# Kernel optimization log

Hardware: AMD Instinct MI355X
Metric: run time of the kernel (lower is better)

The kernel has to match this reference:

```python
import jax, jax.numpy as jnp
import numpy as np

N = 4096      # number of mesh points
H = 64        # hidden_dim
K = 15        # k_neighbors
E = 32768     # explicit input edges


def _knn_edges(points, k):
    # dense pairwise squared distances [N,N]; exclude self via +inf diagonal
    sq = jnp.sum(points * points, axis=1)
    d2 = sq[:, None] - 2.0 * (points @ points.T) + sq[None, :]
    n = points.shape[0]
    d2 = d2.at[jnp.arange(n), jnp.arange(n)].set(jnp.inf)
    _, idx = jax.lax.top_k(-d2, k)              # [N,k] nearest neighbor ids
    src = jnp.repeat(jnp.arange(n), k)          # node i
    dst = idx.reshape(-1)                       # its neighbors
    return src, dst


def setup_inputs() -> dict:
    key = jax.random.key(0)
    ks = jax.random.split(key, 8)
    points = jax.random.normal(ks[0], (N, 3), jnp.float32)
    features = jax.random.normal(ks[1], (N, H), jnp.float32)
    edge_index = jax.random.randint(ks[2], (2, E), 0, N)

    def lin(k, fin, fout):
        k1, k2 = jax.random.split(k)
        s = 1.0 / np.sqrt(fin)
        W = jax.random.uniform(k1, (fout, fin), jnp.float32, -s, s)
        b = jax.random.uniform(k2, (fout,), jnp.float32, -s, s)
        return W, b

    W_theta, b_theta = lin(ks[3], 3, H)
    W_phi, b_phi = lin(ks[4], H, H)
    W_q, b_q = lin(ks[5], H, H)
    W_k, b_k = lin(ks[6], H, H)
    return dict(points=points, features=features, edge_index=edge_index,
                W_theta=W_theta, b_theta=b_theta, W_phi=W_phi, b_phi=b_phi,
                W_q=W_q, b_q=b_q, W_k=W_k, b_k=b_k)


def reference(points, features, edge_index, W_theta, b_theta, W_phi, b_phi,
              W_q, b_q, W_k, b_k):
    n = points.shape[0]
    # extended edge list = explicit edges + KNN edges (src = node, dst = neighbor)
    src_knn, dst_knn = _knn_edges(points, K)
    src = jnp.concatenate([edge_index[0], src_knn])
    dst = jnp.concatenate([edge_index[1], dst_knn])

    # per-node max-pooled edge MLP: max_j W_theta(p_j - p_i), then ReLU(W_phi(.))
    diff = points[dst] - points[src]                     # [M,3]
    h = diff @ W_theta.T + b_theta                       # [M,H]
    max_feat = jax.ops.segment_max(h, src, num_segments=n)  # [N,H] (every node has >=K nbrs)
    dev = jax.nn.relu(max_feat @ W_phi.T + b_phi)        # [N,H]

    # edge softmax attention: attn[i,j] = exp(q_j . k_i) / sum_{j' in N(i)} exp(q_j' . k_i)
    q = dev @ W_q.T + b_q
    kk = dev @ W_k.T + b_k
    e = jnp.exp(jnp.sum(q[dst] * kk[src], axis=-1))      # [M]
    denom = jax.ops.segment_sum(e, src, num_segments=n)  # [N]
    attn = jnp.zeros((n, n), e.dtype).at[src, dst].set(e / denom[src])

    # dense adjacency and sparsified adjacency A_s = attn @ A @ attn^T
    A = jnp.zeros((n, n), points.dtype).at[src, dst].set(1.0)
    A_s = attn @ A @ attn.T
    return A_s
```

## Files before the change

kernel.cpp:

```cpp
#include <hip/hip_runtime.h>

#define NN 4096
#define HD 64
#define KNB 15
#define NE 32768
#define NM (NE + NN*KNB)
#define W64 (NN/64)
#define RB 4
#define MAXH 96
#define NCH (NN/64)
#define TDP 65
#define QPC (MAXH/4)

typedef unsigned long long u64;
typedef unsigned int u32;

__device__ __forceinline__ u32 fmapu(float f) {
  int i = __float_as_int(f);
  return (u32)(i ^ ((i >> 31) | 0x80000000));
}

__device__ __forceinline__ u64 shfl_xor_u64(u64 v, int off) {
  int lo = __shfl_xor((int)(v & 0xFFFFFFFFull), off, 64);
  int hi = __shfl_xor((int)(v >> 32), off, 64);
  return ((u64)(u32)hi << 32) | (u32)lo;
}

__device__ __forceinline__ float dot64(const float* __restrict__ a,
                                       const float* __restrict__ b) {
  const float4* a4 = (const float4*)a;
  const float4* b4 = (const float4*)b;
  float s = 0.f;
#pragma unroll
  for (int t = 0; t < 16; ++t) {
    float4 x = a4[t], y = b4[t];
    s = fmaf(x.x, y.x, s); s = fmaf(x.y, y.y, s);
    s = fmaf(x.z, y.z, s); s = fmaf(x.w, y.w, s);
  }
  return s;
}

__device__ __forceinline__ void edge_decode(int m, const int* __restrict__ ei,
                                            const int* __restrict__ knn_idx,
                                            int& s, int& d) {
  if (m < NE) { s = ei[m]; d = ei[NE + m]; }
  else { int mm = m - NE; s = mm / KNB; d = knn_idx[mm]; }
}

__global__ __launch_bounds__(256) void knn_kernel(const float* __restrict__ pts,
                                                  int* __restrict__ knn_idx,
                                                  u64* __restrict__ bR,
                                                  u32* __restrict__ zero_base,
                                                  int zero_n) {
  int zi = blockIdx.x * 256 + threadIdx.x;
  if (zi < zero_n) zero_base[zi] = 0u;

  __shared__ u64 sm[KNB][4];
  __shared__ u64 s_mask[64];
  __shared__ int s_j[KNB];
  int i = blockIdx.x;
  int tid = threadIdx.x;
  int lane = tid & 63, wv = tid >> 6;
  float px = pts[i*3+0], py = pts[i*3+1], pz = pts[i*3+2];
  float sqi = __fadd_rn(__fadd_rn(__fmul_rn(px,px), __fmul_rn(py,py)), __fmul_rn(pz,pz));
  u64 lk[16];
#pragma unroll
  for (int s = 0; s < 16; ++s) {
    int j = s*256 + tid;
    float x = pts[j*3+0], y = pts[j*3+1], z = pts[j*3+2];
    float sqj = __fadd_rn(__fadd_rn(__fmul_rn(x,x), __fmul_rn(y,y)), __fmul_rn(z,z));
    float dot = fmaf(pz, z, fmaf(py, y, __fmul_rn(px, x)));
    float d2 = __fadd_rn(__fsub_rn(sqi, __fmul_rn(2.0f, dot)), sqj);
    u32 key = (j == i) ? 0xFFFFFFFFu : fmapu(d2);
    lk[s] = ((u64)key << 32) | (u32)j;
  }
  u64 lmin = lk[0];
#pragma unroll
  for (int s = 1; s < 16; ++s) lmin = (lk[s] < lmin) ? lk[s] : lmin;

  for (int r = 0; r < KNB; ++r) {
    u64 v = lmin;
#pragma unroll
    for (int off = 32; off >= 1; off >>= 1) {
      u64 o = shfl_xor_u64(v, off);
      if (o < v) v = o;
    }
    if (lane == 0) sm[r][wv] = v;
    __syncthreads();
    u64 bm = sm[r][0];
    if (sm[r][1] < bm) bm = sm[r][1];
    if (sm[r][2] < bm) bm = sm[r][2];
    if (sm[r][3] < bm) bm = sm[r][3];
    int j = (int)(u32)(bm & 0xFFFFFFFFull);
    if (tid == 0) { knn_idx[i*KNB + r] = j; s_j[r] = j; }
    int owner = j & 255, sid = j >> 8;
    if (tid == owner) {
#pragma unroll
      for (int s2 = 0; s2 < 16; ++s2) if (s2 == sid) lk[s2] = ~0ull;
      lmin = lk[0];
#pragma unroll
      for (int s2 = 1; s2 < 16; ++s2) lmin = (lk[s2] < lmin) ? lk[s2] : lmin;
    }
  }
  if (tid < 64) s_mask[tid] = 0ull;
  __syncthreads();
  if (tid < KNB) {
    int j = s_j[tid];
    atomicOr(&s_mask[j >> 6], 1ull << (j & 63));
  }
  __syncthreads();
  if (tid < 64) bR[(size_t)i*W64 + tid] = s_mask[tid];
}

__global__ void bitmap_kernel(const int* __restrict__ ei, u64* __restrict__ bR) {
  int m = blockIdx.x * 256 + threadIdx.x;
  if (m >= NE) return;
  int s = ei[m], d = ei[NE + m];
  atomicOr(&bR[(size_t)s*W64 + (d >> 6)], 1ull << (d & 63));
}

__global__ __launch_bounds__(512) void theta_devqk_kernel(const float* __restrict__ pts,
    const u64* __restrict__ bR, int* __restrict__ deg, uint2* __restrict__ cvT,
    const float* __restrict__ Wt, const float* __restrict__ bt,
    const float* __restrict__ Wp, const float* __restrict__ bp,
    const float* __restrict__ Wq, const float* __restrict__ bq,
    const float* __restrict__ Wk, const float* __restrict__ bk,
    float* __restrict__ qv, float* __restrict__ kv) {
  __shared__ float Wps[HD*TDP], Wqs[HD*TDP], Wks[HD*TDP];
  __shared__ float mf[8][HD];
  __shared__ float dv[8][HD];
  __shared__ int colbuf[8][MAXH];
  int tid = threadIdx.x;
  for (int m = tid; m < HD*HD; m += 512) {
    int row = m >> 6, col = m & 63;
    Wps[row*TDP + col] = Wp[m];
    Wqs[row*TDP + col] = Wq[m];
    Wks[row*TDP + col] = Wk[m];
  }
  int lane = tid & 63, sub = tid >> 6;
  int i = blockIdx.x * 8 + sub;
  u64 word = bR[(size_t)i*W64 + lane];
  int cnt = __popcll(word);
  int x = cnt;
#pragma unroll
  for (int o = 1; o < 64; o <<= 1) {
    int v = __shfl_up(x, o, 64);
    if (lane >= o) x += v;
  }
  int rank = x - cnt;
  int degi = __shfl(x, 63, 64);
  if (lane == 63) deg[i] = x;
  int ci = i >> 6, il = i & 63;
  u32* colTx = (u32*)cvT;
  int slot = rank;
  u64 wtmp = word;
  while (wtmp) {
    int b = __builtin_ctzll(wtmp); wtmp &= wtmp - 1;
    int col = lane*64 + b;
    colbuf[sub][slot] = col;
    colTx[(((size_t)(ci*MAXH + slot) << 6) + il) << 1] = (u32)col;
    ++slot;
  }
  __syncthreads();
  float w0 = Wt[lane*3+0], w1 = Wt[lane*3+1], w2 = Wt[lane*3+2], bb = bt[lane];
  float px = pts[i*3+0], py = pts[i*3+1], pz = pts[i*3+2];
  float m = -INFINITY;
  for (int e = 0; e < degi; ++e) {
    int d = colbuf[sub][e];
    float dx = __fsub_rn(pts[d*3+0], px);
    float dy = __fsub_rn(pts[d*3+1], py);
    float dz = __fsub_rn(pts[d*3+2], pz);
    float t = fmaf(dz, w2, fmaf(dy, w1, __fmul_rn(dx, w0)));
    m = fmaxf(m, __fadd_rn(t, bb));
  }
  mf[sub][lane] = m;
  __syncthreads();
  float a = 0.f;
#pragma unroll
  for (int t = 0; t < HD; ++t) a = fmaf(Wps[lane*TDP + t], mf[sub][t], a);
  float dvv = a + bp[lane];
  dv[sub][lane] = dvv > 0.f ? dvv : 0.f;
  __syncthreads();
  float aq = 0.f, ak = 0.f;
#pragma unroll
  for (int t = 0; t < HD; ++t) {
    float xv = dv[sub][t];
    aq = fmaf(Wqs[lane*TDP + t], xv, aq);
    ak = fmaf(Wks[lane*TDP + t], xv, ak);
  }
  qv[(size_t)i*HD + lane] = aq + bq[lane];
  kv[(size_t)i*HD + lane] = ak + bk[lane];
}

#define DENOM_BLKS ((NM + 255) / 256)
#define ELL_BLKS   (NCH * QPC * 64 / 256)
__global__ void vals_kernel(const int* __restrict__ ei, const int* __restrict__ knn_idx,
    const int* __restrict__ deg,
    const float* __restrict__ qv, const float* __restrict__ kv,
    float* __restrict__ denom, uint2* __restrict__ cvT) {
  if ((int)blockIdx.x < DENOM_BLKS) {
    int m = blockIdx.x * 256 + threadIdx.x;
    if (m >= NM) return;
    int s, d; edge_decode(m, ei, knn_idx, s, d);
    float e = expf(dot64(qv + (size_t)d*HD, kv + (size_t)s*HD));
    atomicAdd(&denom[s], e);
  } else {
    int t = (blockIdx.x - DENOM_BLKS) * 256 + threadIdx.x;
    int cq = t >> 6, jl = t & 63;
    int c = cq / QPC, q = cq - c * QPC;
    int j = c * 64 + jl;
    int s0 = q * 4;
    int dj = deg[j];
    if (s0 >= dj) return;
    float4 kr[16];
    const float4* kp = (const float4*)(kv + (size_t)j*HD);
#pragma unroll
    for (int u = 0; u < 16; ++u) kr[u] = kp[u];
    int nb = dj - s0; if (nb > 4) nb = 4;
#pragma unroll 4
    for (int u = 0; u < nb; ++u) {
      size_t slot = ((size_t)(c*MAXH + s0 + u) << 6) + jl;
      u32 l = ((const u32*)cvT)[slot << 1];
      const float4* qp = (const float4*)(qv + (size_t)l*HD);
      float sc = 0.f;
#pragma unroll
      for (int v = 0; v < 16; ++v) {
        float4 xq = qp[v], yk = kr[v];
        sc = fmaf(xq.x, yk.x, sc); sc = fmaf(xq.y, yk.y, sc);
        sc = fmaf(xq.z, yk.z, sc); sc = fmaf(xq.w, yk.w, sc);
      }
      ((u32*)cvT)[(slot << 1) + 1] = __float_as_uint(expf(sc));
    }
  }
}

__global__ __launch_bounds__(1024, 8) void final_kernel(
    const int* __restrict__ deg, const uint2* __restrict__ cvT,
    const float* __restrict__ denom, float* __restrict__ out) {
  __shared__ float4 T4[NN];
  int tid = threadIdx.x;
  int i0 = blockIdx.x * RB;
  float4 z4 = make_float4(0.f, 0.f, 0.f, 0.f);
  for (int t = tid; t < NN; t += 1024) T4[t] = z4;
  __syncthreads();
  int w = tid >> 6, lane = tid & 63;
  float* Tf = (float*)T4;
  const u32* colTx = (const u32*)cvT;
  {
    int r = w & (RB - 1);
    int i = i0 + r;
    int ci = i >> 6, il = i & 63;
    int degi = deg[i];
    for (int idx = (w >> 2); idx < degi; idx += RB) {
      uint2 e = cvT[((size_t)(ci*MAXH + idx) << 6) + il];
      int k = (int)e.x; float wv = __uint_as_float(e.y);
      int ck = k >> 6, kl = k & 63;
      int degk = deg[k];
      for (int t = lane; t < degk; t += 64) {
        u32 l = colTx[(((size_t)(ck*MAXH + t) << 6) + kl) << 1];
        atomicAdd(&Tf[(int)l * 4 + r], wv);
      }
    }
  }
  __syncthreads();
  float acc[4][RB];
#pragma unroll
  for (int g = 0; g < 4; ++g)
#pragma unroll
    for (int r = 0; r < RB; ++r) acc[g][r] = 0.f;
#pragma unroll
  for (int g = 0; g < 4; ++g) {
    int j = tid + g * 1024;
    int c = j >> 6;
    int dj = deg[j];
    const uint2* p = cvT + ((size_t)(c*MAXH) << 6) + (j & 63);
    int s = 0;
    for (; s + 4 <= dj; s += 4) {
      uint2 e0 = p[(size_t)(s+0) << 6];
      uint2 e1 = p[(size_t)(s+1) << 6];
      uint2 e2 = p[(size_t)(s+2) << 6];
      uint2 e3 = p[(size_t)(s+3) << 6];
      float4 t0 = T4[(int)e0.x];
      float4 t1 = T4[(int)e1.x];
      float4 t2 = T4[(int)e2.x];
      float4 t3 = T4[(int)e3.x];
      float v0 = __uint_as_float(e0.y), v1 = __uint_as_float(e1.y);
      float v2 = __uint_as_float(e2.y), v3 = __uint_as_float(e3.y);
      acc[g][0] = fmaf(v0, t0.x, acc[g][0]); acc[g][1] = fmaf(v0, t0.y, acc[g][1]);
      acc[g][2] = fmaf(v0, t0.z, acc[g][2]); acc[g][3] = fmaf(v0, t0.w, acc[g][3]);
      acc[g][0] = fmaf(v1, t1.x, acc[g][0]); acc[g][1] = fmaf(v1, t1.y, acc[g][1]);
      acc[g][2] = fmaf(v1, t1.z, acc[g][2]); acc[g][3] = fmaf(v1, t1.w, acc[g][3]);
      acc[g][0] = fmaf(v2, t2.x, acc[g][0]); acc[g][1] = fmaf(v2, t2.y, acc[g][1]);
      acc[g][2] = fmaf(v2, t2.z, acc[g][2]); acc[g][3] = fmaf(v2, t2.w, acc[g][3]);
      acc[g][0] = fmaf(v3, t3.x, acc[g][0]); acc[g][1] = fmaf(v3, t3.y, acc[g][1]);
      acc[g][2] = fmaf(v3, t3.z, acc[g][2]); acc[g][3] = fmaf(v3, t3.w, acc[g][3]);
    }
    for (; s < dj; ++s) {
      uint2 e = p[(size_t)s << 6];
      float v = __uint_as_float(e.y);
      float4 tv = T4[(int)e.x];
      acc[g][0] = fmaf(v, tv.x, acc[g][0]);
      acc[g][1] = fmaf(v, tv.y, acc[g][1]);
      acc[g][2] = fmaf(v, tv.z, acc[g][2]);
      acc[g][3] = fmaf(v, tv.w, acc[g][3]);
    }
  }
  float rden[RB];
#pragma unroll
  for (int r = 0; r < RB; ++r) rden[r] = 1.0f / denom[i0 + r];
#pragma unroll
  for (int g = 0; g < 4; ++g) {
    int j = tid + g * 1024;
    float dj_den = denom[j];
#pragma unroll
    for (int r = 0; r < RB; ++r)
      out[(size_t)(i0 + r) * NN + j] = acc[g][r] * rden[r] / dj_den;
  }
}

extern "C" void kernel_launch(void* const* d_in, const int* in_sizes, int n_in,
                              void* d_out, int out_size, void* d_ws, size_t ws_size,
                              hipStream_t stream) {
  (void)in_sizes; (void)n_in; (void)out_size;
  const float* pts = (const float*)d_in[0];
  const int* ei = (const int*)d_in[2];
  const float* Wt = (const float*)d_in[3];
  const float* bt = (const float*)d_in[4];
  const float* Wp = (const float*)d_in[5];
  const float* bp = (const float*)d_in[6];
  const float* Wq = (const float*)d_in[7];
  const float* bq = (const float*)d_in[8];
  const float* Wk = (const float*)d_in[9];
  const float* bk = (const float*)d_in[10];
  float* out = (float*)d_out;

  char* w = (char*)d_ws;
  u64* bR = (u64*)w;        w += (size_t)NN*W64*8;
  float* denom = (float*)w; w += (size_t)NN*4;
  float* qv = (float*)w;    w += (size_t)NN*HD*4;
  float* kv = (float*)w;    w += (size_t)NN*HD*4;
  int* knn_idx = (int*)w;   w += (size_t)NN*KNB*4;
  int* deg = (int*)w;       w += (size_t)NN*4;
  uint2* cvT = (uint2*)w;   w += (size_t)NCH*MAXH*64*8;
  if ((size_t)(w - (char*)d_ws) > ws_size) return;

  hipLaunchKernelGGL(knn_kernel, dim3(NN), dim3(256), 0, stream,
                     pts, knn_idx, bR, (u32*)denom, NN);
  hipLaunchKernelGGL(bitmap_kernel, dim3((NE+255)/256), dim3(256), 0, stream,
                     ei, bR);
  hipLaunchKernelGGL(theta_devqk_kernel, dim3(NN/8), dim3(512), 0, stream,
                     pts, bR, deg, cvT, Wt, bt, Wp, bp, Wq, bq, Wk, bk, qv, kv);
  hipLaunchKernelGGL(vals_kernel, dim3(DENOM_BLKS + ELL_BLKS), dim3(256), 0, stream,
                     ei, knn_idx, deg, qv, kv, denom, cvT);
  hipLaunchKernelGGL(final_kernel, dim3(NN/RB), dim3(1024), 0, stream,
                     deg, cvT, denom, out);
}
```

Baseline: 172.9 us.

## Run per-wave KNN top-k without barriers, merge by rank, and unroll MLP loops

The KNN selection now has each 64-lane wave extract its own 15 smallest candidates using only shuffles. The four per-wave lists are then merged once with a rank count, which removes the 15 block-wide barriers per node. In the theta/MLP kernel the neighbour gather loop is unrolled by four with int4 index loads and max-tree reduction. The small matvecs use four independent accumulators to break the FMA dependency chains. The trade-off is a different floating-point summation order in the matvecs, plus a little extra merge work and shared memory for the per-wave lists.

```diff
diff --git a/kernel.cpp b/kernel.cpp
--- a/kernel.cpp
+++ b/kernel.cpp
@@ -55,9 +55,8 @@
   int zi = blockIdx.x * 256 + threadIdx.x;
   if (zi < zero_n) zero_base[zi] = 0u;
 
-  __shared__ u64 sm[KNB][4];
+  __shared__ u64 wtop[4][KNB];
   __shared__ u64 s_mask[64];
-  __shared__ int s_j[KNB];
   int i = blockIdx.x;
   int tid = threadIdx.x;
   int lane = tid & 63, wv = tid >> 6;
@@ -85,16 +84,10 @@
       u64 o = shfl_xor_u64(v, off);
       if (o < v) v = o;
     }
-    if (lane == 0) sm[r][wv] = v;
-    __syncthreads();
-    u64 bm = sm[r][0];
-    if (sm[r][1] < bm) bm = sm[r][1];
-    if (sm[r][2] < bm) bm = sm[r][2];
-    if (sm[r][3] < bm) bm = sm[r][3];
-    int j = (int)(u32)(bm & 0xFFFFFFFFull);
-    if (tid == 0) { knn_idx[i*KNB + r] = j; s_j[r] = j; }
-    int owner = j & 255, sid = j >> 8;
-    if (tid == owner) {
+    if (lane == 0) wtop[wv][r] = v;
+    int j = (int)(u32)(v & 0xFFFFFFFFull);
+    int owner = j & 63, sid = j >> 8;
+    if (lane == owner) {
 #pragma unroll
       for (int s2 = 0; s2 < 16; ++s2) if (s2 == sid) lk[s2] = ~0ull;
       lmin = lk[0];
@@ -104,9 +97,19 @@
   }
   if (tid < 64) s_mask[tid] = 0ull;
   __syncthreads();
-  if (tid < KNB) {
-    int j = s_j[tid];
-    atomicOr(&s_mask[j >> 6], 1ull << (j & 63));
+  if (tid < 4*KNB) {
+    u64 x = wtop[tid / KNB][tid % KNB];
+    int rank = 0;
+#pragma unroll
+    for (int w2 = 0; w2 < 4; ++w2)
+#pragma unroll
+      for (int r2 = 0; r2 < KNB; ++r2)
+        rank += (wtop[w2][r2] < x) ? 1 : 0;
+    if (rank < KNB) {
+      int j = (int)(u32)(x & 0xFFFFFFFFull);
+      knn_idx[i*KNB + rank] = j;
+      atomicOr(&s_mask[j >> 6], 1ull << (j & 63));
+    }
   }
   __syncthreads();
   if (tid < 64) bR[(size_t)i*W64 + tid] = s_mask[tid];
@@ -165,7 +168,26 @@
   float w0 = Wt[lane*3+0], w1 = Wt[lane*3+1], w2 = Wt[lane*3+2], bb = bt[lane];
   float px = pts[i*3+0], py = pts[i*3+1], pz = pts[i*3+2];
   float m = -INFINITY;
-  for (int e = 0; e < degi; ++e) {
+  int e = 0;
+  for (; e + 4 <= degi; e += 4) {
+    int4 d4 = *(const int4*)&colbuf[sub][e];
+    float dx0 = __fsub_rn(pts[d4.x*3+0], px), dy0 = __fsub_rn(pts[d4.x*3+1], py),
+          dz0 = __fsub_rn(pts[d4.x*3+2], pz);
+    float dx1 = __fsub_rn(pts[d4.y*3+0], px), dy1 = __fsub_rn(pts[d4.y*3+1], py),
+          dz1 = __fsub_rn(pts[d4.y*3+2], pz);
+    float dx2 = __fsub_rn(pts[d4.z*3+0], px), dy2 = __fsub_rn(pts[d4.z*3+1], py),
+          dz2 = __fsub_rn(pts[d4.z*3+2], pz);
+    float dx3 = __fsub_rn(pts[d4.w*3+0], px), dy3 = __fsub_rn(pts[d4.w*3+1], py),
+          dz3 = __fsub_rn(pts[d4.w*3+2], pz);
+    float t0 = fmaf(dz0, w2, fmaf(dy0, w1, __fmul_rn(dx0, w0)));
+    float t1 = fmaf(dz1, w2, fmaf(dy1, w1, __fmul_rn(dx1, w0)));
+    float t2 = fmaf(dz2, w2, fmaf(dy2, w1, __fmul_rn(dx2, w0)));
+    float t3 = fmaf(dz3, w2, fmaf(dy3, w1, __fmul_rn(dx3, w0)));
+    float m01 = fmaxf(__fadd_rn(t0, bb), __fadd_rn(t1, bb));
+    float m23 = fmaxf(__fadd_rn(t2, bb), __fadd_rn(t3, bb));
+    m = fmaxf(m, fmaxf(m01, m23));
+  }
+  for (; e < degi; ++e) {
     int d = colbuf[sub][e];
     float dx = __fsub_rn(pts[d*3+0], px);
     float dy = __fsub_rn(pts[d*3+1], py);
@@ -175,21 +197,35 @@
   }
   mf[sub][lane] = m;
   __syncthreads();
-  float a = 0.f;
-#pragma unroll
-  for (int t = 0; t < HD; ++t) a = fmaf(Wps[lane*TDP + t], mf[sub][t], a);
-  float dvv = a + bp[lane];
-  dv[sub][lane] = dvv > 0.f ? dvv : 0.f;
-  __syncthreads();
-  float aq = 0.f, ak = 0.f;
-#pragma unroll
-  for (int t = 0; t < HD; ++t) {
-    float xv = dv[sub][t];
-    aq = fmaf(Wqs[lane*TDP + t], xv, aq);
-    ak = fmaf(Wks[lane*TDP + t], xv, ak);
-  }
-  qv[(size_t)i*HD + lane] = aq + bq[lane];
-  kv[(size_t)i*HD + lane] = ak + bk[lane];
+  {
+    float a0 = 0.f, a1 = 0.f, a2 = 0.f, a3 = 0.f;
+#pragma unroll
+    for (int t = 0; t < HD; t += 4) {
+      a0 = fmaf(Wps[lane*TDP + t    ], mf[sub][t    ], a0);
+      a1 = fmaf(Wps[lane*TDP + t + 1], mf[sub][t + 1], a1);
+      a2 = fmaf(Wps[lane*TDP + t + 2], mf[sub][t + 2], a2);
+      a3 = fmaf(Wps[lane*TDP + t + 3], mf[sub][t + 3], a3);
+    }
+    float dvv = ((a0 + a1) + (a2 + a3)) + bp[lane];
+    dv[sub][lane] = dvv > 0.f ? dvv : 0.f;
+  }
+  __syncthreads();
+  float q0 = 0.f, q1 = 0.f, q2 = 0.f, q3 = 0.f;
+  float k0 = 0.f, k1 = 0.f, k2 = 0.f, k3 = 0.f;
+#pragma unroll
+  for (int t = 0; t < HD; t += 4) {
+    float x0 = dv[sub][t], x1 = dv[sub][t+1], x2 = dv[sub][t+2], x3 = dv[sub][t+3];
+    q0 = fmaf(Wqs[lane*TDP + t    ], x0, q0);
+    q1 = fmaf(Wqs[lane*TDP + t + 1], x1, q1);
+    q2 = fmaf(Wqs[lane*TDP + t + 2], x2, q2);
+    q3 = fmaf(Wqs[lane*TDP + t + 3], x3, q3);
+    k0 = fmaf(Wks[lane*TDP + t    ], x0, k0);
+    k1 = fmaf(Wks[lane*TDP + t + 1], x1, k1);
+    k2 = fmaf(Wks[lane*TDP + t + 2], x2, k2);
+    k3 = fmaf(Wks[lane*TDP + t + 3], x3, k3);
+  }
+  qv[(size_t)i*HD + lane] = ((q0 + q1) + (q2 + q3)) + bq[lane];
+  kv[(size_t)i*HD + lane] = ((k0 + k1) + (k2 + k3)) + bk[lane];
 }
 
 #define DENOM_BLKS ((NM + 255) / 256)
```

After: 184.3 us. 1.07x slower.
